# Kernel tuning notes

Hardware: AMD Instinct MI355X
Metric: run time of the kernel (lower is better)

Reference implementation:

```python
import jax, jax.numpy as jnp
import numpy as np

DIM = 2048
N_HEADS = 32
N_KV_HEADS = 8
HEAD_DIM = DIM // N_HEADS  # 64
N_REP = N_HEADS // N_KV_HEADS  # 4
BSZ = 2
SEQ = 2048


def setup_inputs() -> dict:
    key = jax.random.key(0)
    ks = jax.random.split(key, 7)
    s = 0.02
    return {
        "x": jax.random.normal(ks[0], (BSZ, SEQ, DIM), dtype=jnp.float32),
        "freqs_cos": jnp.cos(jnp.outer(jnp.arange(SEQ, dtype=jnp.float32),
                                       1.0 / (10000.0 ** (jnp.arange(0, HEAD_DIM, 2, dtype=jnp.float32) / HEAD_DIM)))),
        "freqs_sin": jnp.sin(jnp.outer(jnp.arange(SEQ, dtype=jnp.float32),
                                       1.0 / (10000.0 ** (jnp.arange(0, HEAD_DIM, 2, dtype=jnp.float32) / HEAD_DIM)))),
        "wq": jax.random.normal(ks[1], (DIM, N_HEADS * HEAD_DIM), dtype=jnp.float32) * s,
        "wk": jax.random.normal(ks[2], (DIM, N_KV_HEADS * HEAD_DIM), dtype=jnp.float32) * s,
        "wv": jax.random.normal(ks[3], (DIM, N_KV_HEADS * HEAD_DIM), dtype=jnp.float32) * s,
        "wo": jax.random.normal(ks[4], (N_HEADS * HEAD_DIM, DIM), dtype=jnp.float32) * s,
    }


def _apply_rope(t, cos, sin):
    # t: [b, s, h, hd]; cos/sin: [s, hd/2] -> broadcast [1, s, 1, hd/2]
    tr = t.reshape(t.shape[:-1] + (HEAD_DIM // 2, 2))
    t_r, t_i = tr[..., 0], tr[..., 1]
    c = cos[None, :, None, :]
    s = sin[None, :, None, :]
    out_r = t_r * c - t_i * s
    out_i = t_r * s + t_i * c
    return jnp.stack([out_r, out_i], axis=-1).reshape(t.shape)


def reference(x, freqs_cos, freqs_sin, wq, wk, wv, wo):
    b, s, _ = x.shape
    xq = (x @ wq).reshape(b, s, N_HEADS, HEAD_DIM)
    xk = (x @ wk).reshape(b, s, N_KV_HEADS, HEAD_DIM)
    xv = (x @ wv).reshape(b, s, N_KV_HEADS, HEAD_DIM)

    xq = _apply_rope(xq, freqs_cos, freqs_sin)
    xk = _apply_rope(xk, freqs_cos, freqs_sin)

    # GQA: group query heads over kv heads instead of materializing repeated KV
    # xq -> [b, kv_heads, n_rep, s, hd]
    q = xq.transpose(0, 2, 1, 3).reshape(b, N_KV_HEADS, N_REP, s, HEAD_DIM)
    k = xk.transpose(0, 2, 1, 3)  # [b, kv, s, hd]
    v = xv.transpose(0, 2, 1, 3)  # [b, kv, s, hd]

    scale = 1.0 / jnp.sqrt(jnp.asarray(HEAD_DIM, dtype=x.dtype))
    scores = jnp.einsum("bgrqd,bgkd->bgrqk", q, k) * scale  # [b,kv,rep,s,s]
    causal = jnp.tril(jnp.ones((s, s), dtype=bool))
    scores = jnp.where(causal[None, None, None], scores, jnp.finfo(scores.dtype).min)
    probs = jax.nn.softmax(scores, axis=-1)
    out = jnp.einsum("bgrqk,bgkd->bgrqd", probs, v)  # [b,kv,rep,s,hd]
    out = out.reshape(b, N_HEADS, s, HEAD_DIM).transpose(0, 2, 1, 3).reshape(b, s, N_HEADS * HEAD_DIM)
    return out @ wo
```

## Files before the change

### kernel.cpp

```cpp
#include <hip/hip_runtime.h>

typedef unsigned short u16;
typedef unsigned int u32;
typedef __bf16 bf16x4 __attribute__((ext_vector_type(4)));
typedef __bf16 bf16x8 __attribute__((ext_vector_type(8)));
typedef float f32x4 __attribute__((ext_vector_type(4)));
typedef u32 u32x2 __attribute__((ext_vector_type(2)));
typedef short s16x4 __attribute__((ext_vector_type(4)));

struct __align__(4) U16x2 { u16 x, y; };
struct __align__(8) U16x4 { u16 x, y, z, w; };

#define DEV static __device__ __forceinline__

extern "C" __device__ float __ocml_exp2_f32(float);

DEV u16 f2bf(float f) {
  __bf16 h = (__bf16)f;
  return __builtin_bit_cast(u16, h);
}
DEV float bf2f(u16 u) { return __uint_as_float(((u32)u) << 16); }

DEV void gload16(const void* g, void* l) {
  __builtin_amdgcn_global_load_lds((const __attribute__((address_space(1))) char*)g,
                                   (__attribute__((address_space(3))) char*)l, 16, 0, 0);
}

DEV f32x4 mfma16(bf16x8 a, bf16x8 b, f32x4 c) {
  return __builtin_amdgcn_mfma_f32_16x16x32_bf16(a, b, c, 0, 0, 0);
}

DEV f32x4 mfma_k16(s16x4 a, s16x4 b, f32x4 c) {
#if __has_builtin(__builtin_amdgcn_mfma_f32_16x16x16bf16_1k)
  return __builtin_amdgcn_mfma_f32_16x16x16bf16_1k(a, b, c, 0, 0, 0);
#else
  f32x4 d;
  asm("v_mfma_f32_16x16x16_bf16 %0, %1, %2, %3"
      : "=v"(d)
      : "v"(a), "v"(b), "0"(c));
  return d;
#endif
}

__global__ __launch_bounds__(256) void cvt_x(const float* __restrict__ x, u16* __restrict__ xb) {
  int i = blockIdx.x * 256 + threadIdx.x;
  float4 v = ((const float4*)x)[i];
  U16x4 o;
  o.x = f2bf(v.x); o.y = f2bf(v.y); o.z = f2bf(v.z); o.w = f2bf(v.w);
  ((U16x4*)xb)[i] = o;
}

__global__ __launch_bounds__(256) void tconv(const float* __restrict__ src, u16* __restrict__ dst,
                                             int C, int nOff, int ldd) {
  __shared__ float t[32][33];
  int bx = blockIdx.x, by = blockIdx.y;
  int tx = threadIdx.x, ty = threadIdx.y;
#pragma unroll
  for (int j = 0; j < 4; ++j)
    t[ty + 8 * j][tx] = src[(size_t)(by * 32 + ty + 8 * j) * C + bx * 32 + tx];
  __syncthreads();
#pragma unroll
  for (int j = 0; j < 4; ++j)
    dst[(size_t)(nOff + bx * 32 + ty + 8 * j) * ldd + by * 32 + tx] = f2bf(t[tx][ty + 8 * j]);
}

__global__ __launch_bounds__(256) void vtrans(const u16* __restrict__ qkv, u16* __restrict__ Vt) {
  __shared__ u16 t[32][33];
  int bx = blockIdx.x, by = blockIdx.y, bz = blockIdx.z;
  int tx = threadIdx.x, ty = threadIdx.y;
  int b = bz >> 3, kh = bz & 7;
  const u16* src = qkv + (size_t)(b * 2048 + bx * 32) * 3072 + 2560 + kh * 64 + by * 32;
#pragma unroll
  for (int j = 0; j < 4; ++j) t[ty + 8 * j][tx] = src[(size_t)(ty + 8 * j) * 3072 + tx];
  __syncthreads();
  u16* dst = Vt + ((size_t)bz * 64 + by * 32) * 2048 + bx * 32;
#pragma unroll
  for (int j = 0; j < 4; ++j) dst[(size_t)(ty + 8 * j) * 2048 + tx] = t[tx][ty + 8 * j];
}

__global__ __launch_bounds__(256) void rope_qk(const u16* __restrict__ qkv,
                                               const float* __restrict__ fc,
                                               const float* __restrict__ fs,
                                               u16* __restrict__ Qo, u16* __restrict__ Ko) {
  int t = blockIdx.x * 256 + threadIdx.x;
  int d2 = t & 31;
  int rest = t >> 5;
  int h40 = rest % 40;
  int bs = rest / 40;
  int s = bs & 2047;
  int b = bs >> 11;
  const u16* src;
  u16* dst;
  float qscale;
  if (h40 < 32) {
    src = qkv + (size_t)bs * 3072 + h40 * 64 + 2 * d2;
    dst = Qo + (((size_t)(b * 32 + h40) * 2048 + s) * 64 + 2 * d2);
    qscale = 0.18033688011112042f;
  } else {
    int kh = h40 - 32;
    src = qkv + (size_t)bs * 3072 + 2048 + kh * 64 + 2 * d2;
    dst = Ko + (((size_t)(b * 8 + kh) * 2048 + s) * 64 + 2 * d2);
    qscale = 1.0f;
  }
  U16x2 v = *(const U16x2*)src;
  float xr = bf2f(v.x), xi = bf2f(v.y);
  float c = fc[s * 32 + d2] * qscale, sn = fs[s * 32 + d2] * qscale;
  U16x2 o;
  o.x = f2bf(xr * c - xi * sn);
  o.y = f2bf(xr * sn + xi * c);
  *(U16x2*)dst = o;
}

template <typename OutT>
__global__ __launch_bounds__(256, 2) void gemm_bt(const u16* __restrict__ A,
                                                  const u16* __restrict__ BT,
                                                  OutT* __restrict__ C,
                                                  int M, int N, int K) {
  __shared__ __align__(16) char smem[65536];
  const int tid = threadIdx.x;
  const int lane = tid & 63;
  const int wm = (tid >> 7) & 1, wn = (tid >> 6) & 1;
  const int tm = blockIdx.y, tn = blockIdx.x;
  const int Kb = K * 2;

  f32x4 acc[4][4];
#pragma unroll
  for (int i = 0; i < 4; ++i)
#pragma unroll
    for (int j = 0; j < 4; ++j) acc[i][j] = (f32x4){0.f, 0.f, 0.f, 0.f};

  const char* Ag = (const char*)A + (size_t)tm * 128 * Kb;
  const char* Bg = (const char*)BT + (size_t)tn * 128 * Kb;

  auto stage = [&](int buf, int t) {
#pragma unroll
    for (int i = 0; i < 4; ++i) {
      int vt = i * 256 + tid;
      int row = vt >> 3;
      int cb = (((vt & 7) << 4) ^ ((row & 7) << 4));
      gload16(Ag + (size_t)row * Kb + t * 128 + cb, smem + buf * 16384 + vt * 16);
      gload16(Bg + (size_t)row * Kb + t * 128 + cb, smem + 32768 + buf * 16384 + vt * 16);
    }
  };

  stage(0, 0);
  int cur = 0;
  const int NT = K >> 6;
  for (int t = 0; t < NT; ++t) {
    __syncthreads();
    if (t + 1 < NT) stage(cur ^ 1, t + 1);
    const char* As = smem + cur * 16384;
    const char* Bs = smem + 32768 + cur * 16384;
#pragma unroll
    for (int ks = 0; ks < 2; ++ks) {
      bf16x8 a[4], b[4];
#pragma unroll
      for (int mf = 0; mf < 4; ++mf) {
        int row = wm * 64 + mf * 16 + (lane & 15);
        int cb = (ks * 64 + ((lane >> 4) << 4)) ^ ((row & 7) << 4);
        a[mf] = *(const bf16x8*)(As + row * 128 + cb);
      }
#pragma unroll
      for (int nf = 0; nf < 4; ++nf) {
        int row = wn * 64 + nf * 16 + (lane & 15);
        int cb = (ks * 64 + ((lane >> 4) << 4)) ^ ((row & 7) << 4);
        b[nf] = *(const bf16x8*)(Bs + row * 128 + cb);
      }
#pragma unroll
      for (int mf = 0; mf < 4; ++mf)
#pragma unroll
        for (int nf = 0; nf < 4; ++nf) acc[mf][nf] = mfma16(a[mf], b[nf], acc[mf][nf]);
    }
    cur ^= 1;
  }
#pragma unroll
  for (int mf = 0; mf < 4; ++mf) {
    int row0 = tm * 128 + wm * 64 + mf * 16 + ((lane >> 4) << 2);
#pragma unroll
    for (int nf = 0; nf < 4; ++nf) {
      int col = tn * 128 + wn * 64 + nf * 16 + (lane & 15);
#pragma unroll
      for (int r = 0; r < 4; ++r) {
        float v = acc[mf][nf][r];
        if constexpr (sizeof(OutT) == 4)
          C[(size_t)(row0 + r) * N + col] = v;
        else
          C[(size_t)(row0 + r) * N + col] = f2bf(v);
      }
    }
  }
}

__global__ __launch_bounds__(128, 2) void attn(const u16* __restrict__ Q,
                                               const u16* __restrict__ Kt,
                                               const u16* __restrict__ Vt,
                                               u16* __restrict__ O) {
  __shared__ __align__(16) char smem[32768];

  const int tid = threadIdx.x, lane = tid & 63, w = tid >> 6;
  const int q15 = lane & 15, g = lane >> 4;
  const int bx = blockIdx.x, h = blockIdx.y, b = blockIdx.z;
  const int kh = h >> 2;

  const char* Kg = (const char*)(Kt + ((size_t)(b * 8 + kh) * 2048 * 64));
  const char* Vg = (const char*)(Vt + ((size_t)(b * 8 + kh) * 64 * 2048));

  auto stageKV = [&](int buf, int kt) {
#pragma unroll
    for (int i = 0; i < 4; ++i) {
      int vt = i * 128 + tid;
      int row = vt >> 3;
      int cb = (((vt & 7) << 4) ^ ((row & 7) << 4));
      gload16(Kg + (size_t)(kt * 64 + row) * 128 + cb, smem + buf * 8192 + vt * 16);
      gload16(Vg + (size_t)row * 4096 + kt * 128 + cb, smem + 16384 + buf * 8192 + vt * 16);
    }
  };

#pragma unroll 1
  for (int ph = 0; ph < 2; ++ph) {
    const int qb = ph ? (31 - bx) : bx;
    const char* Qg = (const char*)(Q + (((size_t)(b * 32 + h) * 2048 + qb * 64) * 64));
    u16* Og = O + ((size_t)(b * 2048 + qb * 64) * 2048 + h * 64);

    bf16x8 qf[2][2];
#pragma unroll
    for (int mf2 = 0; mf2 < 2; ++mf2)
#pragma unroll
      for (int ks = 0; ks < 2; ++ks) {
        int row = w * 32 + mf2 * 16 + q15;
        qf[mf2][ks] = *(const bf16x8*)(Qg + row * 128 + ks * 64 + (g << 4));
      }

    f32x4 acc[2][4];
#pragma unroll
    for (int i = 0; i < 2; ++i)
#pragma unroll
      for (int j = 0; j < 4; ++j) acc[i][j] = (f32x4){0.f, 0.f, 0.f, 0.f};
    float m_r[2] = {-1e30f, -1e30f}, l_r[2] = {0.f, 0.f};

    __syncthreads();
    stageKV(0, 0);
    int cur = 0;
    const int nkt = qb + 1;
    for (int kt = 0; kt < nkt; ++kt) {
      __syncthreads();
      if (kt + 1 < nkt) stageKV(cur ^ 1, kt + 1);
      const char* Ks = smem + cur * 8192;
      const char* Vs = smem + 16384 + cur * 8192;

      f32x4 st[2][4];
#pragma unroll
      for (int i = 0; i < 2; ++i)
#pragma unroll
        for (int j = 0; j < 4; ++j) st[i][j] = (f32x4){0.f, 0.f, 0.f, 0.f};
      __builtin_amdgcn_s_setprio(1);
#pragma unroll
      for (int ks = 0; ks < 2; ++ks) {
        bf16x8 kf[4];
#pragma unroll
        for (int nf = 0; nf < 4; ++nf) {
          int row = nf * 16 + q15;
          int cb = (ks * 64 + (g << 4)) ^ ((row & 7) << 4);
          kf[nf] = *(const bf16x8*)(Ks + row * 128 + cb);
        }
#pragma unroll
        for (int mf2 = 0; mf2 < 2; ++mf2)
#pragma unroll
          for (int nf = 0; nf < 4; ++nf)
            st[mf2][nf] = mfma16(kf[nf], qf[mf2][ks], st[mf2][nf]);
      }
      __builtin_amdgcn_s_setprio(0);

      if (kt >= qb) {
#pragma unroll
        for (int mf2 = 0; mf2 < 2; ++mf2) {
          int qg = qb * 64 + w * 32 + mf2 * 16 + q15;
#pragma unroll
          for (int nf = 0; nf < 4; ++nf)
#pragma unroll
            for (int r = 0; r < 4; ++r) {
              int kg = kt * 64 + nf * 16 + 4 * g + r;
              if (kg > qg) st[mf2][nf][r] = -1e30f;
            }
        }
      }

      s16x4 pa[2][4];
#pragma unroll
      for (int mf2 = 0; mf2 < 2; ++mf2) {
        float vm = st[mf2][0][0];
#pragma unroll
        for (int nf = 0; nf < 4; ++nf)
#pragma unroll
          for (int r = 0; r < 4; ++r) vm = fmaxf(vm, st[mf2][nf][r]);
        vm = fmaxf(vm, __shfl_xor(vm, 16, 64));
        vm = fmaxf(vm, __shfl_xor(vm, 32, 64));

        const bool rescale = !__all(vm - m_r[mf2] <= 8.0f);
        if (rescale) {
          float mn = fmaxf(m_r[mf2], vm);
          float cr = __ocml_exp2_f32(m_r[mf2] - mn);
          m_r[mf2] = mn;
          l_r[mf2] *= cr;
          float cra[4];
#pragma unroll
          for (int r = 0; r < 4; ++r) cra[r] = __shfl(cr, 4 * g + r, 64);
#pragma unroll
          for (int nf = 0; nf < 4; ++nf)
#pragma unroll
            for (int r = 0; r < 4; ++r) acc[mf2][nf][r] *= cra[r];
        }

        float vs = 0.f;
        const float mn = m_r[mf2];
#pragma unroll
        for (int nf = 0; nf < 4; ++nf) {
          float p0 = __ocml_exp2_f32(st[mf2][nf][0] - mn);
          float p1 = __ocml_exp2_f32(st[mf2][nf][1] - mn);
          float p2 = __ocml_exp2_f32(st[mf2][nf][2] - mn);
          float p3 = __ocml_exp2_f32(st[mf2][nf][3] - mn);
          vs += (p0 + p1) + (p2 + p3);
          u32x2 pk;
          pk.x = (u32)f2bf(p0) | ((u32)f2bf(p1) << 16);
          pk.y = (u32)f2bf(p2) | ((u32)f2bf(p3) << 16);
          pa[mf2][nf] = __builtin_bit_cast(s16x4, pk);
        }
        vs += __shfl_xor(vs, 16, 64);
        vs += __shfl_xor(vs, 32, 64);
        l_r[mf2] += vs;
      }

#pragma unroll
      for (int ksl = 0; ksl < 4; ++ksl) {
        s16x4 vb[4];
#pragma unroll
        for (int nfd = 0; nfd < 4; ++nfd) {
          int row = nfd * 16 + q15;
          int chunk = (2 * ksl + (g >> 1)) ^ (row & 7);
          vb[nfd] = *(const s16x4*)(Vs + row * 128 + (chunk << 4) + ((g & 1) << 3));
        }
        __builtin_amdgcn_s_setprio(1);
#pragma unroll
        for (int mf2 = 0; mf2 < 2; ++mf2)
#pragma unroll
          for (int nfd = 0; nfd < 4; ++nfd)
            acc[mf2][nfd] = mfma_k16(pa[mf2][ksl], vb[nfd], acc[mf2][nfd]);
        __builtin_amdgcn_s_setprio(0);
      }
      cur ^= 1;
    }

#pragma unroll
    for (int mf2 = 0; mf2 < 2; ++mf2) {
      float la[4];
#pragma unroll
      for (int r = 0; r < 4; ++r) la[r] = __shfl(l_r[mf2], 4 * g + r, 64);
#pragma unroll
      for (int r = 0; r < 4; ++r) {
        int row = w * 32 + mf2 * 16 + 4 * g + r;
        float li = 1.f / la[r];
#pragma unroll
        for (int nf = 0; nf < 4; ++nf)
          Og[(size_t)row * 2048 + nf * 16 + q15] = f2bf(acc[mf2][nf][r] * li);
      }
    }
  }
}

extern "C" void kernel_launch(void* const* d_in, const int* in_sizes, int n_in,
                              void* d_out, int out_size, void* d_ws, size_t ws_size,
                              hipStream_t stream) {
  const float* x = (const float*)d_in[0];
  const float* fc = (const float*)d_in[1];
  const float* fs = (const float*)d_in[2];
  const float* wq = (const float*)d_in[3];
  const float* wk = (const float*)d_in[4];
  const float* wv = (const float*)d_in[5];
  const float* wo = (const float*)d_in[6];
  float* out = (float*)d_out;
  char* ws = (char*)d_ws;

  u16* xb    = (u16*)(ws);
  u16* qkv   = (u16*)(ws + 16777216);
  u16* woT   = (u16*)(ws + 41943040);
  u16* wqkvT = (u16*)(ws + 50331648);
  u16* Kbuf  = (u16*)(ws + 50331648);
  u16* Vtb   = (u16*)(ws + 54525952);
  u16* Qbuf = xb;
  u16* Obuf = qkv;

  dim3 tb(32, 8);
  cvt_x<<<dim3(8192), dim3(256), 0, stream>>>(x, xb);
  tconv<<<dim3(64, 64), tb, 0, stream>>>(wq, wqkvT, 2048, 0, 2048);
  tconv<<<dim3(16, 64), tb, 0, stream>>>(wk, wqkvT, 512, 2048, 2048);
  tconv<<<dim3(16, 64), tb, 0, stream>>>(wv, wqkvT, 512, 2560, 2048);
  tconv<<<dim3(64, 64), tb, 0, stream>>>(wo, woT, 2048, 0, 2048);
  gemm_bt<u16><<<dim3(24, 32), dim3(256), 0, stream>>>(xb, wqkvT, qkv, 4096, 3072, 2048);
  rope_qk<<<dim3(20480), dim3(256), 0, stream>>>(qkv, fc, fs, Qbuf, Kbuf);
  vtrans<<<dim3(64, 2, 16), tb, 0, stream>>>(qkv, Vtb);
  attn<<<dim3(16, 32, 2), dim3(128), 0, stream>>>(Qbuf, Kbuf, Vtb, Obuf);
  gemm_bt<float><<<dim3(16, 32), dim3(256), 0, stream>>>(Obuf, woT, out, 4096, 2048, 2048);
}
```

Measured before the change: 230.8 us.

## Restructure attention into 32-row tiles with paired query tiles sharing KV loads

The attention kernel now processes two 32-row query tiles (a late and an early one) in one pass over the KV tiles, so each K/V tile staged in LDS serves both. The KV tile shrinks to 32 keys, shared memory is halved, and occupancy is raised to four blocks per SM with twice as many blocks. The V transpose kernel permutes columns so one 16-byte LDS read supplies both k16 MFMA operands. exp2 switches to the hardware builtin. This adds more loop iterations and barriers per key, and smaller MFMA tiles per wave.

```diff
diff --git a/kernel.cpp b/kernel.cpp
--- a/kernel.cpp
+++ b/kernel.cpp
@@ -6,6 +6,7 @@
 typedef __bf16 bf16x8 __attribute__((ext_vector_type(8)));
 typedef float f32x4 __attribute__((ext_vector_type(4)));
 typedef u32 u32x2 __attribute__((ext_vector_type(2)));
+typedef u32 u32x4 __attribute__((ext_vector_type(4)));
 typedef short s16x4 __attribute__((ext_vector_type(4)));
 
 struct __align__(4) U16x2 { u16 x, y; };
@@ -14,12 +15,18 @@
 #define DEV static __device__ __forceinline__
 
 extern "C" __device__ float __ocml_exp2_f32(float);
+#if __has_builtin(__builtin_amdgcn_exp2f)
+#define EXP2(x) __builtin_amdgcn_exp2f(x)
+#else
+#define EXP2(x) __ocml_exp2_f32(x)
+#endif
 
 DEV u16 f2bf(float f) {
   __bf16 h = (__bf16)f;
   return __builtin_bit_cast(u16, h);
 }
 DEV float bf2f(u16 u) { return __uint_as_float(((u32)u) << 16); }
+DEV u32 pk2bf(float lo, float hi) { return (u32)f2bf(lo) | ((u32)f2bf(hi) << 16); }
 
 DEV void gload16(const void* g, void* l) {
   __builtin_amdgcn_global_load_lds((const __attribute__((address_space(1))) char*)g,
@@ -74,8 +81,9 @@
   for (int j = 0; j < 4; ++j) t[ty + 8 * j][tx] = src[(size_t)(ty + 8 * j) * 3072 + tx];
   __syncthreads();
   u16* dst = Vt + ((size_t)bz * 64 + by * 32) * 2048 + bx * 32;
-#pragma unroll
-  for (int j = 0; j < 4; ++j) dst[(size_t)(ty + 8 * j) * 2048 + tx] = t[tx][ty + 8 * j];
+  int pc = ((tx & 15) >> 2) * 8 + ((tx >> 4) << 2) + (tx & 3);
+#pragma unroll
+  for (int j = 0; j < 4; ++j) dst[(size_t)(ty + 8 * j) * 2048 + pc] = t[tx][ty + 8 * j];
 }
 
 __global__ __launch_bounds__(256) void rope_qk(const u16* __restrict__ qkv,
@@ -191,178 +199,193 @@
   }
 }
 
-__global__ __launch_bounds__(128, 2) void attn(const u16* __restrict__ Q,
+__global__ __launch_bounds__(128, 4) void attn(const u16* __restrict__ Q,
                                                const u16* __restrict__ Kt,
                                                const u16* __restrict__ Vt,
                                                u16* __restrict__ O) {
-  __shared__ __align__(16) char smem[32768];
+  __shared__ __align__(16) char smem[16384];
 
   const int tid = threadIdx.x, lane = tid & 63, w = tid >> 6;
   const int q15 = lane & 15, g = lane >> 4;
   const int bx = blockIdx.x, h = blockIdx.y, b = blockIdx.z;
   const int kh = h >> 2;
-
+  const int QT0 = 63 - bx, QT1 = bx;
+
+  const char* Qg = (const char*)(Q + ((size_t)(b * 32 + h) * 2048) * 64);
   const char* Kg = (const char*)(Kt + ((size_t)(b * 8 + kh) * 2048 * 64));
   const char* Vg = (const char*)(Vt + ((size_t)(b * 8 + kh) * 64 * 2048));
 
+  bf16x8 qf0[2], qf1[2];
+#pragma unroll
+  for (int ks = 0; ks < 2; ++ks) {
+    int r0 = QT0 * 32 + w * 16 + q15;
+    int r1 = QT1 * 32 + w * 16 + q15;
+    qf0[ks] = *(const bf16x8*)(Qg + (size_t)r0 * 128 + ks * 64 + (g << 4));
+    qf1[ks] = *(const bf16x8*)(Qg + (size_t)r1 * 128 + ks * 64 + (g << 4));
+  }
+
+  f32x4 acc0[4], acc1[4];
+#pragma unroll
+  for (int j = 0; j < 4; ++j) {
+    acc0[j] = (f32x4){0.f, 0.f, 0.f, 0.f};
+    acc1[j] = (f32x4){0.f, 0.f, 0.f, 0.f};
+  }
+  float m0 = -1e30f, m1 = -1e30f, l0 = 0.f, l1 = 0.f;
+  const f32x4 FZ = (f32x4){0.f, 0.f, 0.f, 0.f};
+
   auto stageKV = [&](int buf, int kt) {
 #pragma unroll
-    for (int i = 0; i < 4; ++i) {
+    for (int i = 0; i < 2; ++i) {
       int vt = i * 128 + tid;
-      int row = vt >> 3;
-      int cb = (((vt & 7) << 4) ^ ((row & 7) << 4));
-      gload16(Kg + (size_t)(kt * 64 + row) * 128 + cb, smem + buf * 8192 + vt * 16);
-      gload16(Vg + (size_t)row * 4096 + kt * 128 + cb, smem + 16384 + buf * 8192 + vt * 16);
+      int r = vt >> 3, ck = vt & 7;
+      gload16(Kg + (size_t)(kt * 32 + r) * 128 + (((ck ^ r) & 7) << 4),
+              smem + buf * 8192 + vt * 16);
+      int d = vt >> 2, cv = vt & 3;
+      gload16(Vg + (size_t)d * 4096 + kt * 64 + (((cv ^ (d >> 1)) & 3) << 4),
+              smem + buf * 8192 + 4096 + vt * 16);
     }
   };
 
-#pragma unroll 1
-  for (int ph = 0; ph < 2; ++ph) {
-    const int qb = ph ? (31 - bx) : bx;
-    const char* Qg = (const char*)(Q + (((size_t)(b * 32 + h) * 2048 + qb * 64) * 64));
-    u16* Og = O + ((size_t)(b * 2048 + qb * 64) * 2048 + h * 64);
-
-    bf16x8 qf[2][2];
-#pragma unroll
-    for (int mf2 = 0; mf2 < 2; ++mf2)
-#pragma unroll
-      for (int ks = 0; ks < 2; ++ks) {
-        int row = w * 32 + mf2 * 16 + q15;
-        qf[mf2][ks] = *(const bf16x8*)(Qg + row * 128 + ks * 64 + (g << 4));
-      }
-
-    f32x4 acc[2][4];
-#pragma unroll
-    for (int i = 0; i < 2; ++i)
-#pragma unroll
-      for (int j = 0; j < 4; ++j) acc[i][j] = (f32x4){0.f, 0.f, 0.f, 0.f};
-    float m_r[2] = {-1e30f, -1e30f}, l_r[2] = {0.f, 0.f};
-
+  stageKV(0, 0);
+  int cur = 0;
+  const int nkt = QT0 + 1;
+  for (int kt = 0; kt < nkt; ++kt) {
     __syncthreads();
-    stageKV(0, 0);
-    int cur = 0;
-    const int nkt = qb + 1;
-    for (int kt = 0; kt < nkt; ++kt) {
-      __syncthreads();
-      if (kt + 1 < nkt) stageKV(cur ^ 1, kt + 1);
-      const char* Ks = smem + cur * 8192;
-      const char* Vs = smem + 16384 + cur * 8192;
-
-      f32x4 st[2][4];
-#pragma unroll
-      for (int i = 0; i < 2; ++i)
-#pragma unroll
-        for (int j = 0; j < 4; ++j) st[i][j] = (f32x4){0.f, 0.f, 0.f, 0.f};
+    if (kt + 1 < nkt) stageKV(cur ^ 1, kt + 1);
+    const char* Ks = smem + cur * 8192;
+    const char* Vs = smem + cur * 8192 + 4096;
+    const bool la = (kt <= QT1);
+
+    bf16x8 kf[2][2];
+#pragma unroll
+    for (int ks = 0; ks < 2; ++ks)
+#pragma unroll
+      for (int nf = 0; nf < 2; ++nf) {
+        int r = nf * 16 + q15;
+        int c = (4 * ks + g) ^ (r & 7);
+        kf[ks][nf] = *(const bf16x8*)(Ks + r * 128 + (c << 4));
+      }
+
+    f32x4 st0[2], st1[2];
+    __builtin_amdgcn_s_setprio(1);
+#pragma unroll
+    for (int nf = 0; nf < 2; ++nf) {
+      st0[nf] = mfma16(kf[0][nf], qf0[0], FZ);
+      st0[nf] = mfma16(kf[1][nf], qf0[1], st0[nf]);
+    }
+    if (la) {
+#pragma unroll
+      for (int nf = 0; nf < 2; ++nf) {
+        st1[nf] = mfma16(kf[0][nf], qf1[0], FZ);
+        st1[nf] = mfma16(kf[1][nf], qf1[1], st1[nf]);
+      }
+    }
+    __builtin_amdgcn_s_setprio(0);
+
+    if (kt == QT0) {
+      int qg = QT0 * 32 + w * 16 + q15;
+#pragma unroll
+      for (int nf = 0; nf < 2; ++nf)
+#pragma unroll
+        for (int r = 0; r < 4; ++r) {
+          int kg = kt * 32 + nf * 16 + 4 * g + r;
+          if (kg > qg) st0[nf][r] = -1e30f;
+        }
+    }
+    if (la && kt == QT1) {
+      int qg = QT1 * 32 + w * 16 + q15;
+#pragma unroll
+      for (int nf = 0; nf < 2; ++nf)
+#pragma unroll
+        for (int r = 0; r < 4; ++r) {
+          int kg = kt * 32 + nf * 16 + 4 * g + r;
+          if (kg > qg) st1[nf][r] = -1e30f;
+        }
+    }
+
+    s16x4 pa0[2], pa1[2];
+#pragma unroll
+    for (int t = 0; t < 2; ++t) {
+      if (t == 1 && !la) break;
+      f32x4* st = (t == 0) ? st0 : st1;
+      float& m_r = (t == 0) ? m0 : m1;
+      float& l_r = (t == 0) ? l0 : l1;
+      f32x4* accT = (t == 0) ? acc0 : acc1;
+      s16x4* pa = (t == 0) ? pa0 : pa1;
+
+      float vm = fmaxf(fmaxf(fmaxf(st[0][0], st[0][1]), fmaxf(st[0][2], st[0][3])),
+                       fmaxf(fmaxf(st[1][0], st[1][1]), fmaxf(st[1][2], st[1][3])));
+      vm = fmaxf(vm, __shfl_xor(vm, 16, 64));
+      vm = fmaxf(vm, __shfl_xor(vm, 32, 64));
+      const bool resc = !__all(vm - m_r <= 8.0f);
+      if (resc) {
+        float mn = fmaxf(m_r, vm);
+        float cr = EXP2(m_r - mn);
+        m_r = mn;
+        l_r *= cr;
+        float cra[4];
+#pragma unroll
+        for (int r = 0; r < 4; ++r) cra[r] = __shfl(cr, 4 * g + r, 64);
+#pragma unroll
+        for (int nfd = 0; nfd < 4; ++nfd)
+#pragma unroll
+          for (int r = 0; r < 4; ++r) accT[nfd][r] *= cra[r];
+      }
+      float vs = 0.f;
+#pragma unroll
+      for (int nf = 0; nf < 2; ++nf) {
+        float p0 = EXP2(st[nf][0] - m_r);
+        float p1 = EXP2(st[nf][1] - m_r);
+        float p2 = EXP2(st[nf][2] - m_r);
+        float p3 = EXP2(st[nf][3] - m_r);
+        vs += (p0 + p1) + (p2 + p3);
+        u32x2 pk;
+        pk.x = pk2bf(p0, p1);
+        pk.y = pk2bf(p2, p3);
+        pa[nf] = __builtin_bit_cast(s16x4, pk);
+      }
+      vs += __shfl_xor(vs, 16, 64);
+      vs += __shfl_xor(vs, 32, 64);
+      l_r += vs;
+    }
+
+#pragma unroll
+    for (int nfd = 0; nfd < 4; ++nfd) {
+      int d = nfd * 16 + q15;
+      int c = (g ^ (d >> 1)) & 3;
+      bf16x8 wv = *(const bf16x8*)(Vs + d * 64 + (c << 4));
+      u32x4 W = __builtin_bit_cast(u32x4, wv);
+      u32x2 wlo, whi;
+      wlo.x = W.x; wlo.y = W.y; whi.x = W.z; whi.y = W.w;
+      s16x4 v0 = __builtin_bit_cast(s16x4, wlo);
+      s16x4 v1 = __builtin_bit_cast(s16x4, whi);
       __builtin_amdgcn_s_setprio(1);
-#pragma unroll
-      for (int ks = 0; ks < 2; ++ks) {
-        bf16x8 kf[4];
-#pragma unroll
-        for (int nf = 0; nf < 4; ++nf) {
-          int row = nf * 16 + q15;
-          int cb = (ks * 64 + (g << 4)) ^ ((row & 7) << 4);
-          kf[nf] = *(const bf16x8*)(Ks + row * 128 + cb);
-        }
-#pragma unroll
-        for (int mf2 = 0; mf2 < 2; ++mf2)
-#pragma unroll
-          for (int nf = 0; nf < 4; ++nf)
-            st[mf2][nf] = mfma16(kf[nf], qf[mf2][ks], st[mf2][nf]);
+      acc0[nfd] = mfma_k16(pa0[0], v0, acc0[nfd]);
+      acc0[nfd] = mfma_k16(pa0[1], v1, acc0[nfd]);
+      if (la) {
+        acc1[nfd] = mfma_k16(pa1[0], v0, acc1[nfd]);
+        acc1[nfd] = mfma_k16(pa1[1], v1, acc1[nfd]);
       }
       __builtin_amdgcn_s_setprio(0);
-
-      if (kt >= qb) {
-#pragma unroll
-        for (int mf2 = 0; mf2 < 2; ++mf2) {
-          int qg = qb * 64 + w * 32 + mf2 * 16 + q15;
-#pragma unroll
-          for (int nf = 0; nf < 4; ++nf)
-#pragma unroll
-            for (int r = 0; r < 4; ++r) {
-              int kg = kt * 64 + nf * 16 + 4 * g + r;
-              if (kg > qg) st[mf2][nf][r] = -1e30f;
-            }
-        }
-      }
-
-      s16x4 pa[2][4];
-#pragma unroll
-      for (int mf2 = 0; mf2 < 2; ++mf2) {
-        float vm = st[mf2][0][0];
-#pragma unroll
-        for (int nf = 0; nf < 4; ++nf)
-#pragma unroll
-          for (int r = 0; r < 4; ++r) vm = fmaxf(vm, st[mf2][nf][r]);
-        vm = fmaxf(vm, __shfl_xor(vm, 16, 64));
-        vm = fmaxf(vm, __shfl_xor(vm, 32, 64));
-
-        const bool rescale = !__all(vm - m_r[mf2] <= 8.0f);
-        if (rescale) {
-          float mn = fmaxf(m_r[mf2], vm);
-          float cr = __ocml_exp2_f32(m_r[mf2] - mn);
-          m_r[mf2] = mn;
-          l_r[mf2] *= cr;
-          float cra[4];
-#pragma unroll
-          for (int r = 0; r < 4; ++r) cra[r] = __shfl(cr, 4 * g + r, 64);
-#pragma unroll
-          for (int nf = 0; nf < 4; ++nf)
-#pragma unroll
-            for (int r = 0; r < 4; ++r) acc[mf2][nf][r] *= cra[r];
-        }
-
-        float vs = 0.f;
-        const float mn = m_r[mf2];
-#pragma unroll
-        for (int nf = 0; nf < 4; ++nf) {
-          float p0 = __ocml_exp2_f32(st[mf2][nf][0] - mn);
-          float p1 = __ocml_exp2_f32(st[mf2][nf][1] - mn);
-          float p2 = __ocml_exp2_f32(st[mf2][nf][2] - mn);
-          float p3 = __ocml_exp2_f32(st[mf2][nf][3] - mn);
-          vs += (p0 + p1) + (p2 + p3);
-          u32x2 pk;
-          pk.x = (u32)f2bf(p0) | ((u32)f2bf(p1) << 16);
-          pk.y = (u32)f2bf(p2) | ((u32)f2bf(p3) << 16);
-          pa[mf2][nf] = __builtin_bit_cast(s16x4, pk);
-        }
-        vs += __shfl_xor(vs, 16, 64);
-        vs += __shfl_xor(vs, 32, 64);
-        l_r[mf2] += vs;
-      }
-
-#pragma unroll
-      for (int ksl = 0; ksl < 4; ++ksl) {
-        s16x4 vb[4];
-#pragma unroll
-        for (int nfd = 0; nfd < 4; ++nfd) {
-          int row = nfd * 16 + q15;
-          int chunk = (2 * ksl + (g >> 1)) ^ (row & 7);
-          vb[nfd] = *(const s16x4*)(Vs + row * 128 + (chunk << 4) + ((g & 1) << 3));
-        }
-        __builtin_amdgcn_s_setprio(1);
-#pragma unroll
-        for (int mf2 = 0; mf2 < 2; ++mf2)
-#pragma unroll
-          for (int nfd = 0; nfd < 4; ++nfd)
-            acc[mf2][nfd] = mfma_k16(pa[mf2][ksl], vb[nfd], acc[mf2][nfd]);
-        __builtin_amdgcn_s_setprio(0);
-      }
-      cur ^= 1;
-    }
-
-#pragma unroll
-    for (int mf2 = 0; mf2 < 2; ++mf2) {
-      float la[4];
-#pragma unroll
-      for (int r = 0; r < 4; ++r) la[r] = __shfl(l_r[mf2], 4 * g + r, 64);
-#pragma unroll
-      for (int r = 0; r < 4; ++r) {
-        int row = w * 32 + mf2 * 16 + 4 * g + r;
-        float li = 1.f / la[r];
-#pragma unroll
-        for (int nf = 0; nf < 4; ++nf)
-          Og[(size_t)row * 2048 + nf * 16 + q15] = f2bf(acc[mf2][nf][r] * li);
-      }
+    }
+    cur ^= 1;
+  }
+
+#pragma unroll
+  for (int t = 0; t < 2; ++t) {
+    float l_r = (t == 0) ? l0 : l1;
+    f32x4* accT = (t == 0) ? acc0 : acc1;
+    int qt = (t == 0) ? QT0 : QT1;
+    u16* Og = O + ((size_t)(b * 2048 + qt * 32 + w * 16) * 2048 + h * 64);
+    float la4[4];
+#pragma unroll
+    for (int r = 0; r < 4; ++r) la4[r] = __shfl(l_r, 4 * g + r, 64);
+#pragma unroll
+    for (int r = 0; r < 4; ++r) {
+      float li = 1.f / la4[r];
+#pragma unroll
+      for (int nfd = 0; nfd < 4; ++nfd)
+        Og[(size_t)(4 * g + r) * 2048 + nfd * 16 + q15] = f2bf(accT[nfd][r] * li);
     }
   }
 }
@@ -398,6 +421,6 @@
   gemm_bt<u16><<<dim3(24, 32), dim3(256), 0, stream>>>(xb, wqkvT, qkv, 4096, 3072, 2048);
   rope_qk<<<dim3(20480), dim3(256), 0, stream>>>(qkv, fc, fs, Qbuf, Kbuf);
   vtrans<<<dim3(64, 2, 16), tb, 0, stream>>>(qkv, Vtb);
-  attn<<<dim3(16, 32, 2), dim3(128), 0, stream>>>(Qbuf, Kbuf, Vtb, Obuf);
+  attn<<<dim3(32, 32, 2), dim3(128), 0, stream>>>(Qbuf, Kbuf, Vtb, Obuf);
   gemm_bt<float><<<dim3(16, 32), dim3(256), 0, stream>>>(Obuf, woT, out, 4096, 2048, 2048);
 }
```

Result: faster. 221.3 us (-4.1%).
